# Optimization experiments

Hardware: AMD Instinct MI355X
Metric: run time of the kernel (lower is better)

## Reference

```python
import jax, jax.numpy as jnp
import numpy as np

N, E = 20000, 640000
F_IN, H, T = 64, 256, 64  # in_channels = T, edge_attr dim = T -> EdgeConv MLP in = 3*T


def _lin(key, fan_in, fan_out):
    k1, k2 = jax.random.split(key)
    s = 1.0 / np.sqrt(fan_in)
    W = jax.random.uniform(k1, (fan_in, fan_out), jnp.float32, -s, s)
    b = jax.random.uniform(k2, (fan_out,), jnp.float32, -s, s)
    return W, b


def setup_inputs() -> dict:
    key = jax.random.key(0)
    ks = jax.random.split(key, 12)
    x = jax.random.normal(ks[0], (N, F_IN), jnp.float32)
    edge_index = jax.random.randint(ks[1], (2, E), 0, N, jnp.int32)
    edge_attr = jax.random.normal(ks[2], (E, T), jnp.float32)
    conv1_W, conv1_b = _lin(ks[3], F_IN, H)
    e_W1, e_b1 = _lin(ks[4], 3 * T, H)
    e_W2, e_b2 = _lin(ks[5], H, H)
    conv2_W, conv2_b = _lin(ks[6], 2 * H, H)
    conv3_W, conv3_b = _lin(ks[7], H, F_IN)
    lin1_W, lin1_b = _lin(ks[8], 2 * F_IN, F_IN)
    lin2_W, lin2_b = _lin(ks[9], F_IN, 128)
    lin3_W, lin3_b = _lin(ks[10], 128, 32)
    lin4_W, lin4_b = _lin(ks[11], 32, 2)
    return dict(x=x, edge_index=edge_index, edge_attr=edge_attr,
                conv1_W=conv1_W, conv1_b=conv1_b,
                e_W1=e_W1, e_b1=e_b1, e_W2=e_W2, e_b2=e_b2,
                conv2_W=conv2_W, conv2_b=conv2_b,
                conv3_W=conv3_W, conv3_b=conv3_b,
                lin1_W=lin1_W, lin1_b=lin1_b, lin2_W=lin2_W, lin2_b=lin2_b,
                lin3_W=lin3_W, lin3_b=lin3_b, lin4_W=lin4_W, lin4_b=lin4_b)


def reference(x, edge_index, edge_attr,
              conv1_W, conv1_b, e_W1, e_b1, e_W2, e_b2,
              conv2_W, conv2_b, conv3_W, conv3_b,
              lin1_W, lin1_b, lin2_W, lin2_b, lin3_W, lin3_b, lin4_W, lin4_b):
    n = x.shape[0]
    src, dst = edge_index[0], edge_index[1]
    # GCN symmetric norm with self-loops (deg counted on dst, +1 for self-loop)
    deg = jax.ops.segment_sum(jnp.ones_like(src, jnp.float32), dst, num_segments=n) + 1.0
    dis = jax.lax.rsqrt(deg)

    def gcn(h, W, b):
        hw = h @ W
        msg = hw[src] * (dis[src] * dis[dst])[:, None]
        # self-loop contribution: norm = dis[i]^2
        return jax.ops.segment_sum(msg, dst, num_segments=n) + hw * (dis * dis)[:, None] + b

    out1 = jax.nn.relu(gcn(x, conv1_W, conv1_b))
    # EdgeConv: MLP(cat[x_i, x_j, edge_attr]) with max aggregation onto dst (x_i = target)
    m = jnp.concatenate([x[dst], x[src], edge_attr], axis=1)      # [E, 3T]
    m = jax.nn.relu(m @ e_W1 + e_b1) @ e_W2 + e_b2                 # [E, H]
    agg = jax.ops.segment_max(m, dst, num_segments=n)
    agg = jnp.where(jnp.isfinite(agg), agg, 0.0)                   # nodes with no in-edges
    out_e1 = jax.nn.relu(agg)

    out2 = jax.nn.relu(gcn(jnp.concatenate([out1, out_e1], axis=1), conv2_W, conv2_b))
    out3 = jax.nn.relu(gcn(out2, conv3_W, conv3_b))
    h = jnp.concatenate([x, out3], axis=1)
    h = jax.nn.softplus(h @ lin1_W + lin1_b)
    h = jax.nn.softplus(h @ lin2_W + lin2_b)
    h = jax.nn.softplus(h @ lin3_W + lin3_b)
    h = h @ lin4_W + lin4_b                                        # [N, 2]
    return (h[:, 0], h[:, 1])
```

## Files before the change

### kernel.cpp

```cpp
#include <hip/hip_runtime.h>
#include <stdint.h>

typedef __bf16 bf16x8 __attribute__((ext_vector_type(8)));
typedef float f32x4 __attribute__((ext_vector_type(4)));
typedef unsigned short u16x8 __attribute__((ext_vector_type(8)));
typedef unsigned long long ull_t;
typedef unsigned short ushort_t;

#define DEV __device__ __forceinline__

DEV unsigned short f2bf(float f) {
  __bf16 b = (__bf16)f;
  return __builtin_bit_cast(unsigned short, b);
}

DEV float bf2f(unsigned short b) { return __uint_as_float((unsigned int)b << 16); }

DEV f32x4 zero4() { f32x4 z = {0.f, 0.f, 0.f, 0.f}; return z; }

DEV float softplusf(float v) { return (v > 15.f) ? v : log1pf(expf(v)); }

__global__ void pack_weight(const float* __restrict__ W, unsigned short* __restrict__ P,
                            int K, int Ncols, int permk) {
  int idx = blockIdx.x * 256 + threadIdx.x;
  if (idx >= K * Ncols) return;
  int j = idx & 7;
  int lane = (idx >> 3) & 63;
  int rest = idx >> 9;
  int NT = Ncols >> 4;
  int nt = rest % NT;
  int kt = rest / NT;
  int k = kt * 32 + ((j >> 2) * 16) + ((lane >> 4) * 4) + (j & 3);
  if (permk) k = (k & ~63) | ((k & 3) << 4) | ((k >> 2) & 15);
  int col = nt * 16 + (lane & 15);
  P[idx] = f2bf(W[(size_t)k * Ncols + col]);
}

__global__ void k_cvt_bf16(const float* __restrict__ in, ushort_t* __restrict__ out,
                           int n4) {
  int i = blockIdx.x * 256 + threadIdx.x;
  if (i >= n4) return;
  float4 v = *(const float4*)(in + (size_t)i * 4);
  ushort4 b;
  b.x = f2bf(v.x); b.y = f2bf(v.y); b.z = f2bf(v.z); b.w = f2bf(v.w);
  *(ushort4*)(out + (size_t)i * 4) = b;
}

__global__ void k_deg(const int* __restrict__ dst, int* __restrict__ degi, int E) {
  int i = blockIdx.x * 256 + threadIdx.x;
  if (i < E) atomicAdd(&degi[dst[i]], 1);
}

__global__ void k_dis(const int* __restrict__ degi, float* __restrict__ dis, int n) {
  int i = blockIdx.x * 256 + threadIdx.x;
  if (i < n) dis[i] = rsqrtf((float)degi[i] + 1.0f);
}

__global__ __launch_bounds__(1024) void k_scan(const int* __restrict__ degi,
                                               int* __restrict__ ptr, int n) {
  __shared__ int part[1024];
  const int tid = threadIdx.x;
  const int chunk = (n + 1023) / 1024;
  const int b = tid * chunk;
  const int e2 = min(n, b + chunk);
  int s = 0;
  for (int i = b; i < e2; ++i) s += degi[i];
  part[tid] = s;
  __syncthreads();
  for (int off = 1; off < 1024; off <<= 1) {
    int val = (tid >= off) ? part[tid - off] : 0;
    __syncthreads();
    part[tid] += val;
    __syncthreads();
  }
  int run = (tid == 0) ? 0 : part[tid - 1];
  for (int i = b; i < e2; ++i) {
    ptr[i] = run;
    run += degi[i];
  }
  if (tid == 1023) ptr[n] = run;
}

__global__ void k_fill(const int* __restrict__ srcs, const int* __restrict__ dsts,
                       const int* __restrict__ ptr, const float* __restrict__ dis,
                       int* __restrict__ fillc,
                       int2* __restrict__ sc_s, int* __restrict__ dst_s,
                       int* __restrict__ perm_s, int E) {
  int e = blockIdx.x * 256 + threadIdx.x;
  if (e >= E) return;
  int d = dsts[e];
  int s = srcs[e];
  int pos = ptr[d] + atomicAdd(&fillc[d], 1);
  float c = dis[s] * dis[d];
  sc_s[pos] = make_int2(s, __float_as_int(c));
  dst_s[pos] = d;
  perm_s[pos] = e;
}

template <int COLS, bool FINALIZE, bool INBF16>
__global__ __launch_bounds__(256) void k_gather_agg(
    const void* __restrict__ featv, const int2* __restrict__ sc,
    const int* __restrict__ ptr, const float* __restrict__ dis,
    const void* __restrict__ hwv, const float* __restrict__ bias,
    float* __restrict__ out, int n) {
  constexpr int V = COLS / 64;
  const int v = blockIdx.x * 4 + (threadIdx.x >> 6);
  if (v >= n) return;
  const int lane = threadIdx.x & 63;
  const int beg = ptr[v], end = ptr[v + 1];

  auto loadrow = [&](int s, float* f) {
    if constexpr (INBF16) {
      const ushort_t* feat = (const ushort_t*)featv;
      if constexpr (V == 4) {
        ushort4 u = *(const ushort4*)(feat + (size_t)s * COLS + lane * 4);
        f[0] = bf2f(u.x); f[1] = bf2f(u.y); f[2] = bf2f(u.z); f[3] = bf2f(u.w);
      } else {
        f[0] = bf2f(feat[(size_t)s * COLS + lane]);
      }
    } else {
      const float* feat = (const float*)featv;
      if constexpr (V == 4) {
        float4 q = *(const float4*)(feat + (size_t)s * COLS + lane * 4);
        f[0] = q.x; f[1] = q.y; f[2] = q.z; f[3] = q.w;
      } else {
        f[0] = feat[(size_t)s * COLS + lane];
      }
    }
  };

  float acc[V];
#pragma unroll
  for (int i = 0; i < V; ++i) acc[i] = 0.f;
  const int cnt = end - beg;
  const int2* scp = sc + beg;
  int i = 0;
  for (; i + 4 <= cnt; i += 4) {
    int2 s0 = scp[i], s1 = scp[i + 1], s2 = scp[i + 2], s3 = scp[i + 3];
    float f0[V], f1[V], f2[V], f3[V];
    loadrow(s0.x, f0); loadrow(s1.x, f1); loadrow(s2.x, f2); loadrow(s3.x, f3);
    float c0 = __int_as_float(s0.y), c1 = __int_as_float(s1.y);
    float c2 = __int_as_float(s2.y), c3 = __int_as_float(s3.y);
#pragma unroll
    for (int j = 0; j < V; ++j)
      acc[j] += f0[j] * c0 + f1[j] * c1 + f2[j] * c2 + f3[j] * c3;
  }
  for (; i < cnt; ++i) {
    int2 s0 = scp[i];
    float c0 = __int_as_float(s0.y);
    float f0[V];
    loadrow(s0.x, f0);
#pragma unroll
    for (int j = 0; j < V; ++j) acc[j] += f0[j] * c0;
  }
  float* op = out + (size_t)v * COLS + lane * V;
  if constexpr (FINALIZE) {
    const float dv = dis[v];
    float d2 = dv * dv;
    float h[V];
    if constexpr (INBF16) {
      const ushort_t* hw = (const ushort_t*)hwv;
      if constexpr (V == 4) {
        ushort4 u = *(const ushort4*)(hw + (size_t)v * COLS + lane * 4);
        h[0] = bf2f(u.x); h[1] = bf2f(u.y); h[2] = bf2f(u.z); h[3] = bf2f(u.w);
      } else {
        h[0] = bf2f(hw[(size_t)v * COLS + lane]);
      }
    } else {
      const float* hw = (const float*)hwv;
      if constexpr (V == 4) {
        float4 q = *(const float4*)(hw + (size_t)v * COLS + lane * 4);
        h[0] = q.x; h[1] = q.y; h[2] = q.z; h[3] = q.w;
      } else {
        h[0] = hw[(size_t)v * COLS + lane];
      }
    }
#pragma unroll
    for (int i2 = 0; i2 < V; ++i2)
      acc[i2] = fmaxf(acc[i2] + h[i2] * d2 + bias[lane * V + i2], 0.f);
  }
  if constexpr (V == 4) {
    *(float4*)op = make_float4(acc[0], acc[1], acc[2], acc[3]);
  } else {
    op[0] = acc[0];
  }
}

template <int K, int NOUT, bool COMPOSE, bool RELUBIAS, bool OUTBF16>
__global__ __launch_bounds__(256, 2) void gcn_gemm(
    const float* __restrict__ inA, const float* __restrict__ inB,
    const float* __restrict__ dis,
    const unsigned short* __restrict__ Wp, const float* __restrict__ bias,
    void* __restrict__ outv, int out_stride, int nrows) {
  constexpr int NT = NOUT / 16;
  constexpr int NTW = NOUT / 64;
  __shared__ unsigned short s_in[64 * K];
  const int tid = threadIdx.x;
  const int r0 = blockIdx.x * 64;

  constexpr int C4R = K / 4;
  for (int idx = tid; idx < 64 * C4R; idx += 256) {
    int row = idx / C4R;
    int rem = idx - row * C4R;
    int grow = r0 + row;
    float4 v = make_float4(0.f, 0.f, 0.f, 0.f);
    if (grow < nrows) {
      v = *(const float4*)&inA[(size_t)grow * K + rem * 4];
      if constexpr (COMPOSE) {
        float d = dis[grow];
        d *= d;
        float4 w2 = *(const float4*)&inB[(size_t)grow * K + rem * 4];
        v.x += w2.x * d; v.y += w2.y * d; v.z += w2.z * d; v.w += w2.w * d;
      }
    }
    ushort4 b;
    b.x = f2bf(v.x); b.y = f2bf(v.y); b.z = f2bf(v.z); b.w = f2bf(v.w);
    *(ushort4*)&s_in[row * K + ((rem ^ (row & 7)) * 4)] = b;
  }
  __syncthreads();

  const int lane = tid & 63, wid = tid >> 6;
  const int lr = lane & 15, lg = lane >> 4;
  f32x4 acc[4][NTW];
#pragma unroll
  for (int m = 0; m < 4; ++m)
#pragma unroll
    for (int n2 = 0; n2 < NTW; ++n2) acc[m][n2] = zero4();

#pragma unroll
  for (int kt = 0; kt < K / 32; ++kt) {
    bf16x8 a[4];
#pragma unroll
    for (int m = 0; m < 4; ++m) {
      int rA = m * 16 + lr;
      int c1 = (kt * 8 + lg) ^ (rA & 7);
      int c2 = (kt * 8 + lg + 4) ^ (rA & 7);
      union { bf16x8 v; ull_t q[2]; } u;
      u.q[0] = *(const ull_t*)&s_in[rA * K + c1 * 4];
      u.q[1] = *(const ull_t*)&s_in[rA * K + c2 * 4];
      a[m] = u.v;
    }
#pragma unroll
    for (int n2 = 0; n2 < NTW; ++n2) {
      int nt = wid * NTW + n2;
      bf16x8 b = *(const bf16x8*)&Wp[(((kt * NT + nt) * 64 + lane) * 8)];
#pragma unroll
      for (int m = 0; m < 4; ++m)
        acc[m][n2] = __builtin_amdgcn_mfma_f32_16x16x32_bf16(a[m], b, acc[m][n2], 0, 0, 0);
    }
  }

#pragma unroll
  for (int n2 = 0; n2 < NTW; ++n2) {
    int col = (wid * NTW + n2) * 16 + lr;
    float bv = 0.f;
    if (RELUBIAS) bv = bias[col];
#pragma unroll
    for (int m = 0; m < 4; ++m) {
#pragma unroll
      for (int r = 0; r < 4; ++r) {
        int grow = r0 + m * 16 + lg * 4 + r;
        if (grow < nrows) {
          float v = acc[m][n2][r];
          if (RELUBIAS) v = fmaxf(v + bv, 0.f);
          if constexpr (OUTBF16) {
            ((ushort_t*)outv)[(size_t)grow * out_stride + col] = f2bf(v);
          } else {
            ((float*)outv)[(size_t)grow * out_stride + col] = v;
          }
        }
      }
    }
  }
}

__global__ __launch_bounds__(512, 4) void k_edgeconv(
    const float* __restrict__ x, const float* __restrict__ ea,
    const int2* __restrict__ sc_s, const int* __restrict__ dst_s,
    const int* __restrict__ perm_s,
    const unsigned short* __restrict__ W1p, const float* __restrict__ b1,
    const unsigned short* __restrict__ W2p, const float* __restrict__ b2,
    float* __restrict__ h2, int E) {
  __shared__ unsigned short s_buf[256 * 136];
  __shared__ int s_src[128], s_dst[128], s_perm[128];
  __shared__ ull_t s_mask[2];
  const int tid = threadIdx.x;
  const int e0 = blockIdx.x * 128;
  const int lane = tid & 63, wid = tid >> 6;
  if (tid < 128) {
    int e = e0 + tid;
    s_src[tid] = (e < E) ? sc_s[e].x : 0;
    s_dst[tid] = (e < E) ? dst_s[e] : 0;
    s_perm[tid] = (e < E) ? perm_s[e] : 0;
  }
  __syncthreads();
  if (wid < 2) {
    int r = wid * 64 + lane;
    bool chg = (r > 0) && (s_dst[r] != s_dst[r - 1]);
    ull_t m = __ballot(chg);
    if (lane == 0) s_mask[wid] = m;
  }
#pragma unroll
  for (int seg = 0; seg < 3; ++seg) {
#pragma unroll
    for (int it = 0; it < 4; ++it) {
      int idx = it * 512 + tid;
      int ei = idx >> 4;
      int q = idx & 15;
      const float* row;
      if (seg == 0) row = x + (unsigned)s_dst[ei] * 64u;
      else if (seg == 1) row = x + (unsigned)s_src[ei] * 64u;
      else row = ea + (unsigned)s_perm[ei] * 64u;
      float4 v = make_float4(0.f, 0.f, 0.f, 0.f);
      if (e0 + ei < E) v = *(const float4*)(row + q * 4);
      ushort4 b;
      b.x = f2bf(v.x); b.y = f2bf(v.y); b.z = f2bf(v.z); b.w = f2bf(v.w);
      int chunk = (seg * 16 + q) ^ (ei & 7);
      *(ushort4*)&s_buf[ei * 192 + chunk * 4] = b;
    }
  }
  __syncthreads();

  const int wr = wid >> 2;
  const int wc = wid & 3;
  const int lr = lane & 15, lg = lane >> 4;
  f32x4 acc[4][4];
#pragma unroll
  for (int m = 0; m < 4; ++m)
#pragma unroll
    for (int n2 = 0; n2 < 4; ++n2) acc[m][n2] = zero4();

#pragma unroll
  for (int kt = 0; kt < 6; ++kt) {
    bf16x8 a[4];
#pragma unroll
    for (int m = 0; m < 4; ++m) {
      int rA = wr * 64 + m * 16 + lr;
      int rr = rA & 7;
      union { bf16x8 v; ull_t q[2]; } u;
      u.q[0] = *(const ull_t*)&s_buf[rA * 192 + ((kt * 8 + lg) ^ rr) * 4];
      u.q[1] = *(const ull_t*)&s_buf[rA * 192 + ((kt * 8 + lg + 4) ^ rr) * 4];
      a[m] = u.v;
    }
#pragma unroll
    for (int n2 = 0; n2 < 4; ++n2) {
      int nt = wc * 4 + n2;
      bf16x8 b = *(const bf16x8*)&W1p[(((kt * 16 + nt) * 64 + lane) * 8)];
#pragma unroll
      for (int m = 0; m < 4; ++m)
        acc[m][n2] = __builtin_amdgcn_mfma_f32_16x16x32_bf16(a[m], b, acc[m][n2], 0, 0, 0);
    }
  }
  __syncthreads();

  {
    float b1v[4];
#pragma unroll
    for (int n2 = 0; n2 < 4; ++n2) b1v[n2] = b1[(wc * 4 + n2) * 16 + lr];
#pragma unroll
    for (int m = 0; m < 4; ++m) {
#pragma unroll
      for (int r = 0; r < 4; ++r) {
        int row = wr * 64 + m * 16 + lg * 4 + r;
        union { ushort_t h[4]; ull_t q; } pk;
        pk.h[0] = f2bf(fmaxf(acc[m][0][r] + b1v[0], 0.f));
        pk.h[1] = f2bf(fmaxf(acc[m][1][r] + b1v[1], 0.f));
        pk.h[2] = f2bf(fmaxf(acc[m][2][r] + b1v[2], 0.f));
        pk.h[3] = f2bf(fmaxf(acc[m][3][r] + b1v[3], 0.f));
        int chunk = (wc * 16 + lr) ^ (row & 7);
        *(ull_t*)&s_buf[row * 256 + chunk * 4] = pk.q;
      }
    }
  }
  __syncthreads();

#pragma unroll
  for (int m = 0; m < 4; ++m)
#pragma unroll
    for (int n2 = 0; n2 < 4; ++n2) acc[m][n2] = zero4();
#pragma unroll
  for (int kt = 0; kt < 8; ++kt) {
    bf16x8 a[4];
#pragma unroll
    for (int m = 0; m < 4; ++m) {
      int rA = wr * 64 + m * 16 + lr;
      int rr = rA & 7;
      union { bf16x8 v; ull_t q[2]; } u;
      u.q[0] = *(const ull_t*)&s_buf[rA * 256 + ((kt * 8 + lg) ^ rr) * 4];
      u.q[1] = *(const ull_t*)&s_buf[rA * 256 + ((kt * 8 + lg + 4) ^ rr) * 4];
      a[m] = u.v;
    }
#pragma unroll
    for (int n2 = 0; n2 < 4; ++n2) {
      int nt = wc * 4 + n2;
      bf16x8 b = *(const bf16x8*)&W2p[(((kt * 16 + nt) * 64 + lane) * 8)];
#pragma unroll
      for (int m = 0; m < 4; ++m)
        acc[m][n2] = __builtin_amdgcn_mfma_f32_16x16x32_bf16(a[m], b, acc[m][n2], 0, 0, 0);
    }
  }
  __syncthreads();

#pragma unroll
  for (int n2 = 0; n2 < 4; ++n2) {
    int col = (wc * 4 + n2) * 16 + lr;
    float bv = b2[col];
#pragma unroll
    for (int m = 0; m < 4; ++m) {
      int rbase = wr * 64 + m * 16 + lg * 4;
      union { ushort_t h[4]; ull_t q; } pk;
#pragma unroll
      for (int r = 0; r < 4; ++r) {
        int row = rbase + r;
        float v = (e0 + row < E) ? fmaxf(acc[m][n2][r] + bv, 0.f) : 0.f;
        pk.h[r] = f2bf(v);
      }
      *(ull_t*)&s_buf[col * 136 + rbase] = pk.q;
    }
  }
  __syncthreads();

  {
    const int col = tid & 255;
    const int half = tid >> 8;
    const int rbeg = half * 64;
    const ull_t mask = s_mask[half];
    unsigned int run = 0;
    int segstart = rbeg;
#pragma unroll
    for (int i = 0; i < 8; ++i) {
      u16x8 pack = *(const u16x8*)&s_buf[col * 136 + rbeg + i * 8];
#pragma unroll
      for (int r2 = 0; r2 < 8; ++r2) {
        int rloc = i * 8 + r2;
        if ((mask >> rloc) & 1ull) {
          if (run > 0)
            atomicMax((int*)h2 + ((unsigned)s_dst[segstart] * 512u + 256u + col),
                      (int)(run << 16));
          run = 0;
          segstart = rbeg + rloc;
        }
        run = max(run, (unsigned int)pack[r2]);
      }
    }
    if (run > 0)
      atomicMax((int*)h2 + ((unsigned)s_dst[segstart] * 512u + 256u + col),
                (int)(run << 16));
  }
}

__global__ __launch_bounds__(256) void k_head(
    const float* __restrict__ x, const float* __restrict__ out3,
    const float* __restrict__ W1, const float* __restrict__ b1,
    const float* __restrict__ W2, const float* __restrict__ b2,
    const float* __restrict__ W3, const float* __restrict__ b3,
    const float* __restrict__ W4, const float* __restrict__ b4,
    float* __restrict__ out, int n) {
  __shared__ float sW1[128 * 64];
  __shared__ float sW3[128 * 32];
  __shared__ float sW4[32 * 2];
  __shared__ float sb1[64], sb2[128], sb3[32], sb4[2];
  __shared__ float sbuf[4][352];
  const int tid = threadIdx.x;
  for (int i = tid; i < 128 * 64; i += 256) sW1[i] = W1[i];
  for (int i = tid; i < 128 * 32; i += 256) sW3[i] = W3[i];
  if (tid < 64) sW4[tid] = W4[tid];
  if (tid < 64) sb1[tid] = b1[tid];
  if (tid < 128) sb2[tid] = b2[tid];
  if (tid < 32) sb3[tid] = b3[tid];
  if (tid < 2) sb4[tid] = b4[tid];
  __syncthreads();
  const int wid = tid >> 6, lane = tid & 63;
  float* B = sbuf[wid];
  const int per = gridDim.x * 4;
  const int iters = (n + per - 1) / per;
  for (int it = 0; it < iters; ++it) {
    const int node = it * per + blockIdx.x * 4 + wid;
    const bool act = node < n;
    if (act) {
      B[lane] = x[(size_t)node * 64 + lane];
      B[64 + lane] = out3[(size_t)node * 64 + lane];
    }
    __syncthreads();
    if (act) {
      float o = sb1[lane];
#pragma unroll 8
      for (int k = 0; k < 128; ++k) o += B[k] * sW1[k * 64 + lane];
      B[128 + lane] = softplusf(o);
    }
    __syncthreads();
    if (act) {
      float o0 = sb2[lane], o1 = sb2[64 + lane];
#pragma unroll 8
      for (int k = 0; k < 64; ++k) {
        float v = B[128 + k];
        o0 += v * W2[k * 128 + lane];
        o1 += v * W2[k * 128 + 64 + lane];
      }
      B[192 + lane] = softplusf(o0);
      B[256 + lane] = softplusf(o1);
    }
    __syncthreads();
    if (act && lane < 32) {
      float o = sb3[lane];
#pragma unroll 8
      for (int k = 0; k < 128; ++k) o += B[192 + k] * sW3[k * 32 + lane];
      B[320 + lane] = softplusf(o);
    }
    __syncthreads();
    if (act && lane < 2) {
      float o = sb4[lane];
#pragma unroll
      for (int k = 0; k < 32; ++k) o += B[320 + k] * sW4[k * 2 + lane];
      out[(size_t)lane * n + node] = o;
    }
    __syncthreads();
  }
}

static inline size_t alignup(size_t v) { return (v + 255) & ~(size_t)255; }

extern "C" void kernel_launch(void* const* d_in, const int* in_sizes, int n_in,
                              void* d_out, int out_size, void* d_ws, size_t ws_size,
                              hipStream_t stream) {
  const float* x = (const float*)d_in[0];
  const int* ei = (const int*)d_in[1];
  const float* ea = (const float*)d_in[2];
  const float* c1W = (const float*)d_in[3];
  const float* c1b = (const float*)d_in[4];
  const float* eW1 = (const float*)d_in[5];
  const float* eb1 = (const float*)d_in[6];
  const float* eW2 = (const float*)d_in[7];
  const float* eb2 = (const float*)d_in[8];
  const float* c2W = (const float*)d_in[9];
  const float* c2b = (const float*)d_in[10];
  const float* c3W = (const float*)d_in[11];
  const float* c3b = (const float*)d_in[12];
  const float* l1W = (const float*)d_in[13];
  const float* l1b = (const float*)d_in[14];
  const float* l2W = (const float*)d_in[15];
  const float* l2b = (const float*)d_in[16];
  const float* l3W = (const float*)d_in[17];
  const float* l3b = (const float*)d_in[18];
  const float* l4W = (const float*)d_in[19];
  const float* l4b = (const float*)d_in[20];
  const int n = in_sizes[0] / 64;
  const int E = in_sizes[1] / 2;
  const int* srcs = ei;
  const int* dsts = ei + E;

  char* w = (char*)d_ws;
  auto alloc = [&](size_t bytes) {
    char* p = w;
    w += alignup(bytes);
    return p;
  };
  float* dis = (float*)alloc((size_t)n * 4);
  int* degi = (int*)alloc((size_t)n * 4);
  int* ptr = (int*)alloc((size_t)(n + 1) * 4);
  int* fillc = (int*)alloc((size_t)n * 4);
  int2* sc_s = (int2*)alloc((size_t)E * 8);
  int* dst_s = (int*)alloc((size_t)E * 4);
  int* perm_s = (int*)alloc((size_t)E * 4);
  float* agg1 = (float*)alloc((size_t)n * 64 * 4);
  float* h2 = (float*)alloc((size_t)n * 512 * 4);
  ushort_t* hw2b = (ushort_t*)alloc((size_t)n * 256 * 2);
  float* out2 = (float*)alloc((size_t)n * 256 * 4);
  ushort_t* hw3b = (ushort_t*)alloc((size_t)n * 64 * 2);
  float* out3 = (float*)alloc((size_t)n * 64 * 4);
  ushort_t* xb = (ushort_t*)alloc((size_t)n * 64 * 2);
  unsigned short* p_c1 = (unsigned short*)alloc(64 * 256 * 2);
  unsigned short* p_e1 = (unsigned short*)alloc(192 * 256 * 2);
  unsigned short* p_e2 = (unsigned short*)alloc(256 * 256 * 2);
  unsigned short* p_c2 = (unsigned short*)alloc(512 * 256 * 2);
  unsigned short* p_c3 = (unsigned short*)alloc(256 * 64 * 2);

  hipMemsetAsync(degi, 0, (size_t)n * 4, stream);
  hipMemsetAsync(fillc, 0, (size_t)n * 4, stream);
  hipMemsetAsync(h2, 0, (size_t)n * 512 * 4, stream);

  pack_weight<<<(64 * 256) / 256, 256, 0, stream>>>(c1W, p_c1, 64, 256, 0);
  pack_weight<<<(192 * 256) / 256, 256, 0, stream>>>(eW1, p_e1, 192, 256, 0);
  pack_weight<<<(256 * 256) / 256, 256, 0, stream>>>(eW2, p_e2, 256, 256, 1);
  pack_weight<<<(512 * 256) / 256, 256, 0, stream>>>(c2W, p_c2, 512, 256, 0);
  pack_weight<<<(256 * 64) / 256, 256, 0, stream>>>(c3W, p_c3, 256, 64, 0);
  k_cvt_bf16<<<(n * 16 + 255) / 256, 256, 0, stream>>>(x, xb, n * 16);

  k_deg<<<(E + 255) / 256, 256, 0, stream>>>(dsts, degi, E);
  k_dis<<<(n + 255) / 256, 256, 0, stream>>>(degi, dis, n);
  k_scan<<<1, 1024, 0, stream>>>(degi, ptr, n);
  k_fill<<<(E + 255) / 256, 256, 0, stream>>>(srcs, dsts, ptr, dis, fillc,
                                              sc_s, dst_s, perm_s, E);

  const int ablocks = (n + 3) / 4;
  const int gblocks = (n + 63) / 64;

  k_gather_agg<64, false, true><<<ablocks, 256, 0, stream>>>(
      xb, sc_s, ptr, dis, nullptr, nullptr, agg1, n);
  gcn_gemm<64, 256, true, true, false><<<gblocks, 256, 0, stream>>>(
      agg1, x, dis, p_c1, c1b, h2, 512, n);

  k_edgeconv<<<(E + 127) / 128, 512, 0, stream>>>(x, ea, sc_s, dst_s, perm_s,
                                                  p_e1, eb1, p_e2, eb2, h2, E);

  gcn_gemm<512, 256, false, false, true><<<gblocks, 256, 0, stream>>>(
      h2, nullptr, nullptr, p_c2, nullptr, hw2b, 256, n);
  k_gather_agg<256, true, true><<<ablocks, 256, 0, stream>>>(
      hw2b, sc_s, ptr, dis, hw2b, c2b, out2, n);

  gcn_gemm<256, 64, false, false, true><<<gblocks, 256, 0, stream>>>(
      out2, nullptr, nullptr, p_c3, nullptr, hw3b, 64, n);
  k_gather_agg<64, true, true><<<ablocks, 256, 0, stream>>>(
      hw3b, sc_s, ptr, dis, hw3b, c3b, out3, n);

  k_head<<<1250, 256, 0, stream>>>(x, out3, l1W, l1b, l2W, l2b, l3W, l3b, l4W, l4b,
                                   (float*)d_out, n);
}
```

Baseline: 599.8 us.

## Merge prologue kernels and fuse first GCN gather into edgeconv launch

Combines the five weight-pack launches, bf16 conversion and degree counting into one multi-role prologue kernel, and folds the dis computation into the scan. The layer-1 GCN neighbor gather now runs as extra blocks of the edgeconv launch, so gather and edge MLP work share the GPU concurrently, and the conv1 GEMM moves after that launch. This removes several launches and idle tails, at the cost of the gather blocks carrying edgeconv's large shared memory footprint and launch bounds, which may lower their occupancy.

```diff
diff --git a/kernel.cpp b/kernel.cpp
--- a/kernel.cpp
+++ b/kernel.cpp
@@ -20,10 +20,8 @@
 
 DEV float softplusf(float v) { return (v > 15.f) ? v : log1pf(expf(v)); }
 
-__global__ void pack_weight(const float* __restrict__ W, unsigned short* __restrict__ P,
-                            int K, int Ncols, int permk) {
-  int idx = blockIdx.x * 256 + threadIdx.x;
-  if (idx >= K * Ncols) return;
+DEV void pack_dev(const float* __restrict__ W, unsigned short* __restrict__ P,
+                  int Ncols, int permk, int idx) {
   int j = idx & 7;
   int lane = (idx >> 3) & 63;
   int rest = idx >> 9;
@@ -36,35 +34,55 @@
   P[idx] = f2bf(W[(size_t)k * Ncols + col]);
 }
 
-__global__ void k_cvt_bf16(const float* __restrict__ in, ushort_t* __restrict__ out,
-                           int n4) {
-  int i = blockIdx.x * 256 + threadIdx.x;
-  if (i >= n4) return;
-  float4 v = *(const float4*)(in + (size_t)i * 4);
-  ushort4 b;
-  b.x = f2bf(v.x); b.y = f2bf(v.y); b.z = f2bf(v.z); b.w = f2bf(v.w);
-  *(ushort4*)(out + (size_t)i * 4) = b;
-}
-
-__global__ void k_deg(const int* __restrict__ dst, int* __restrict__ degi, int E) {
-  int i = blockIdx.x * 256 + threadIdx.x;
-  if (i < E) atomicAdd(&degi[dst[i]], 1);
-}
-
-__global__ void k_dis(const int* __restrict__ degi, float* __restrict__ dis, int n) {
-  int i = blockIdx.x * 256 + threadIdx.x;
-  if (i < n) dis[i] = rsqrtf((float)degi[i] + 1.0f);
-}
-
-__global__ __launch_bounds__(1024) void k_scan(const int* __restrict__ degi,
-                                               int* __restrict__ ptr, int n) {
+__global__ __launch_bounds__(256) void k_prologue(
+    const float* __restrict__ c1W, unsigned short* __restrict__ p_c1,
+    const float* __restrict__ eW1, unsigned short* __restrict__ p_e1,
+    const float* __restrict__ eW2, unsigned short* __restrict__ p_e2,
+    const float* __restrict__ c2W, unsigned short* __restrict__ p_c2,
+    const float* __restrict__ c3W, unsigned short* __restrict__ p_c3,
+    const float* __restrict__ x, ushort_t* __restrict__ xb,
+    const int* __restrict__ dsts, int* __restrict__ degi,
+    int n4, int E, int nb_cvt) {
+  const int b = blockIdx.x;
+  const int tid = threadIdx.x;
+  if (b < 64) {
+    pack_dev(c1W, p_c1, 256, 0, b * 256 + tid);
+  } else if (b < 256) {
+    pack_dev(eW1, p_e1, 256, 0, (b - 64) * 256 + tid);
+  } else if (b < 512) {
+    pack_dev(eW2, p_e2, 256, 1, (b - 256) * 256 + tid);
+  } else if (b < 1024) {
+    pack_dev(c2W, p_c2, 256, 0, (b - 512) * 256 + tid);
+  } else if (b < 1088) {
+    pack_dev(c3W, p_c3, 64, 0, (b - 1024) * 256 + tid);
+  } else if (b < 1088 + nb_cvt) {
+    int i = (b - 1088) * 256 + tid;
+    if (i < n4) {
+      float4 v = *(const float4*)(x + (size_t)i * 4);
+      ushort4 u;
+      u.x = f2bf(v.x); u.y = f2bf(v.y); u.z = f2bf(v.z); u.w = f2bf(v.w);
+      *(ushort4*)(xb + (size_t)i * 4) = u;
+    }
+  } else {
+    int i = (b - 1088 - nb_cvt) * 256 + tid;
+    if (i < E) atomicAdd(&degi[dsts[i]], 1);
+  }
+}
+
+__global__ __launch_bounds__(1024) void k_scan_dis(const int* __restrict__ degi,
+                                                   int* __restrict__ ptr,
+                                                   float* __restrict__ dis, int n) {
   __shared__ int part[1024];
   const int tid = threadIdx.x;
   const int chunk = (n + 1023) / 1024;
   const int b = tid * chunk;
   const int e2 = min(n, b + chunk);
   int s = 0;
-  for (int i = b; i < e2; ++i) s += degi[i];
+  for (int i = b; i < e2; ++i) {
+    int d = degi[i];
+    dis[i] = rsqrtf((float)d + 1.0f);
+    s += d;
+  }
   part[tid] = s;
   __syncthreads();
   for (int off = 1; off < 1024; off <<= 1) {
@@ -274,19 +292,47 @@
   }
 }
 
-__global__ __launch_bounds__(512, 4) void k_edgeconv(
+__global__ __launch_bounds__(512, 4) void k_fused(
     const float* __restrict__ x, const float* __restrict__ ea,
     const int2* __restrict__ sc_s, const int* __restrict__ dst_s,
     const int* __restrict__ perm_s,
     const unsigned short* __restrict__ W1p, const float* __restrict__ b1,
     const unsigned short* __restrict__ W2p, const float* __restrict__ b2,
-    float* __restrict__ h2, int E) {
+    float* __restrict__ h2, int E, int nbE,
+    const ushort_t* __restrict__ xb, const int* __restrict__ ptr,
+    float* __restrict__ agg1, int n) {
+  const int tid = threadIdx.x;
+  const int lane = tid & 63, wid = tid >> 6;
+
+  if (blockIdx.x >= nbE) {
+    const int v = (blockIdx.x - nbE) * 8 + wid;
+    if (v >= n) return;
+    const int beg = ptr[v], end = ptr[v + 1];
+    float acc = 0.f;
+    const int cnt = end - beg;
+    const int2* scp = sc_s + beg;
+    int i = 0;
+    for (; i + 4 <= cnt; i += 4) {
+      int2 s0 = scp[i], s1 = scp[i + 1], s2 = scp[i + 2], s3 = scp[i + 3];
+      float f0 = bf2f(xb[(size_t)s0.x * 64 + lane]);
+      float f1 = bf2f(xb[(size_t)s1.x * 64 + lane]);
+      float f2 = bf2f(xb[(size_t)s2.x * 64 + lane]);
+      float f3 = bf2f(xb[(size_t)s3.x * 64 + lane]);
+      acc += f0 * __int_as_float(s0.y) + f1 * __int_as_float(s1.y) +
+             f2 * __int_as_float(s2.y) + f3 * __int_as_float(s3.y);
+    }
+    for (; i < cnt; ++i) {
+      int2 s0 = scp[i];
+      acc += bf2f(xb[(size_t)s0.x * 64 + lane]) * __int_as_float(s0.y);
+    }
+    agg1[(size_t)v * 64 + lane] = acc;
+    return;
+  }
+
   __shared__ unsigned short s_buf[256 * 136];
   __shared__ int s_src[128], s_dst[128], s_perm[128];
   __shared__ ull_t s_mask[2];
-  const int tid = threadIdx.x;
   const int e0 = blockIdx.x * 128;
-  const int lane = tid & 63, wid = tid >> 6;
   if (tid < 128) {
     int e = e0 + tid;
     s_src[tid] = (e < E) ? sc_s[e].x : 0;
@@ -579,29 +625,28 @@
   hipMemsetAsync(fillc, 0, (size_t)n * 4, stream);
   hipMemsetAsync(h2, 0, (size_t)n * 512 * 4, stream);
 
-  pack_weight<<<(64 * 256) / 256, 256, 0, stream>>>(c1W, p_c1, 64, 256, 0);
-  pack_weight<<<(192 * 256) / 256, 256, 0, stream>>>(eW1, p_e1, 192, 256, 0);
-  pack_weight<<<(256 * 256) / 256, 256, 0, stream>>>(eW2, p_e2, 256, 256, 1);
-  pack_weight<<<(512 * 256) / 256, 256, 0, stream>>>(c2W, p_c2, 512, 256, 0);
-  pack_weight<<<(256 * 64) / 256, 256, 0, stream>>>(c3W, p_c3, 256, 64, 0);
-  k_cvt_bf16<<<(n * 16 + 255) / 256, 256, 0, stream>>>(x, xb, n * 16);
-
-  k_deg<<<(E + 255) / 256, 256, 0, stream>>>(dsts, degi, E);
-  k_dis<<<(n + 255) / 256, 256, 0, stream>>>(degi, dis, n);
-  k_scan<<<1, 1024, 0, stream>>>(degi, ptr, n);
+  const int n4 = n * 16;
+  const int nb_cvt = (n4 + 255) / 256;
+  const int nb_deg = (E + 255) / 256;
+  k_prologue<<<1088 + nb_cvt + nb_deg, 256, 0, stream>>>(
+      c1W, p_c1, eW1, p_e1, eW2, p_e2, c2W, p_c2, c3W, p_c3,
+      x, xb, dsts, degi, n4, E, nb_cvt);
+
+  k_scan_dis<<<1, 1024, 0, stream>>>(degi, ptr, dis, n);
   k_fill<<<(E + 255) / 256, 256, 0, stream>>>(srcs, dsts, ptr, dis, fillc,
                                               sc_s, dst_s, perm_s, E);
 
   const int ablocks = (n + 3) / 4;
   const int gblocks = (n + 63) / 64;
-
-  k_gather_agg<64, false, true><<<ablocks, 256, 0, stream>>>(
-      xb, sc_s, ptr, dis, nullptr, nullptr, agg1, n);
+  const int nbE = (E + 127) / 128;
+  const int nbG = (n + 7) / 8;
+
+  k_fused<<<nbE + nbG, 512, 0, stream>>>(x, ea, sc_s, dst_s, perm_s,
+                                         p_e1, eb1, p_e2, eb2, h2, E, nbE,
+                                         xb, ptr, agg1, n);
+
   gcn_gemm<64, 256, true, true, false><<<gblocks, 256, 0, stream>>>(
       agg1, x, dis, p_c1, c1b, h2, 512, n);
-
-  k_edgeconv<<<(E + 127) / 128, 512, 0, stream>>>(x, ea, sc_s, dst_s, perm_s,
-                                                  p_e1, eb1, p_e2, eb2, h2, E);
 
   gcn_gemm<512, 256, false, false, true><<<gblocks, 256, 0, stream>>>(
       h2, nullptr, nullptr, p_c2, nullptr, hw2b, 256, n);
```

Result: slower. 617.2 us (+2.9%).
